# Performance work log

Measured on AMD Instinct MI355X. Metric: run time of the kernel, lower is better.

Reference implementation:

```python
import jax, jax.numpy as jnp
import numpy as np

N_NODES = 50000
N_EDGES = 600000
D = 128


def sage_conv(x, edge_index, Wl, bl, Wr):
    # PyG SAGEConv (mean aggr): out = lin_l(mean_{j in N(i)} x_j) + lin_r(x_i)
    src, dst = edge_index[0], edge_index[1]
    msgs = x[src]  # [E, D] gather of neighbor features
    summed = jax.ops.segment_sum(msgs, dst, num_segments=N_NODES)  # [N, D]
    deg = jax.ops.segment_sum(jnp.ones((msgs.shape[0],), x.dtype), dst, num_segments=N_NODES)
    mean = summed / jnp.maximum(deg, 1.0)[:, None]
    return mean @ Wl.T + bl + x @ Wr.T


def setup_inputs() -> dict:
    key = jax.random.key(0)
    ks = jax.random.split(key, 12)
    s = 1.0 / np.sqrt(D)
    inp = {
        "x": jax.random.normal(ks[0], (N_NODES, D), dtype=jnp.float32),
        "edge_index": jax.random.randint(ks[1], (2, N_EDGES), 0, N_NODES, dtype=jnp.int64),
    }
    for i, layer in enumerate([1, 2, 3]):
        inp[f"Wl{layer}"] = jax.random.uniform(ks[2 + 3 * i], (D, D), jnp.float32, -s, s)
        inp[f"bl{layer}"] = jax.random.uniform(ks[3 + 3 * i], (D,), jnp.float32, -s, s)
        inp[f"Wr{layer}"] = jax.random.uniform(ks[4 + 3 * i], (D, D), jnp.float32, -s, s)
    return inp


def reference(x, edge_index, Wl1, bl1, Wr1, Wl2, bl2, Wr2, Wl3, bl3, Wr3):
    h = jax.nn.relu(sage_conv(x, edge_index, Wl1, bl1, Wr1))
    h = jax.nn.relu(sage_conv(h, edge_index, Wl2, bl2, Wr2))
    h = jax.nn.relu(sage_conv(h, edge_index, Wl3, bl3, Wr3))
    return h
```

## Files before the change

### kernel.cpp

```cpp
#include <hip/hip_runtime.h>
#include <hip/hip_bf16.h>
#include <stdint.h>

#define N_NODES 50000
#define N_EDGES 600000
#define DD 128
#define K2 256
#define M_PAD 50048
#define MAXDEG 64
#define NREP 4
#define SEGCAP 16
#define POISON 0xAAAAAAAAu

#define FILL_BLOCKS 2344
#define PREP_BLOCKS 3125

typedef __bf16 bf16x8 __attribute__((ext_vector_type(8)));
typedef float floatx4 __attribute__((ext_vector_type(4)));

__device__ __forceinline__ ushort f2bf(float f) {
    union { float f; uint u; } v; v.f = f;
    uint u = v.u;
    u += 0x7fffu + ((u >> 16) & 1u);
    return (ushort)(u >> 16);
}
__device__ __forceinline__ float bf2f(ushort h) {
    union { uint u; float f; } v; v.u = ((uint)h) << 16;
    return v.f;
}
__device__ __forceinline__ void accum8(float* a, uint4 p) {
    a[0] += bf2f((ushort)(p.x & 0xffffu)); a[1] += bf2f((ushort)(p.x >> 16));
    a[2] += bf2f((ushort)(p.y & 0xffffu)); a[3] += bf2f((ushort)(p.y >> 16));
    a[4] += bf2f((ushort)(p.z & 0xffffu)); a[5] += bf2f((ushort)(p.z >> 16));
    a[6] += bf2f((ushort)(p.w & 0xffffu)); a[7] += bf2f((ushort)(p.w >> 16));
}
__device__ __forceinline__ uint4 packf8(float4 f0, float4 f1) {
    uint4 o;
    o.x = (uint)f2bf(f0.x) | ((uint)f2bf(f0.y) << 16);
    o.y = (uint)f2bf(f0.z) | ((uint)f2bf(f0.w) << 16);
    o.z = (uint)f2bf(f1.x) | ((uint)f2bf(f1.y) << 16);
    o.w = (uint)f2bf(f1.z) | ((uint)f2bf(f1.w) << 16);
    return o;
}


__global__ void k_build(const float* __restrict__ x, ushort* __restrict__ X,
                        uint* __restrict__ cursor, ushort* __restrict__ col,
                        const int* __restrict__ eidx,
                        const float* __restrict__ Wl1, const float* __restrict__ Wr1,
                        const float* __restrict__ Wl2, const float* __restrict__ Wr2,
                        const float* __restrict__ Wl3, const float* __restrict__ Wr3,
                        ushort* __restrict__ Wb) {
    if (blockIdx.x < FILL_BLOCKS) {
        int t = blockIdx.x * 256 + threadIdx.x;
        if (t >= N_EDGES) return;
        int src = eidx[t];
        int dst = eidx[N_EDGES + t];
        int r = t & (NREP - 1);
        uint o = atomicAdd(&cursor[(size_t)dst * NREP + r], 1u) - POISON;
        if (o < SEGCAP) col[dst * MAXDEG + r * SEGCAP + o] = (ushort)src;
    } else {
        int idx = (blockIdx.x - FILL_BLOCKS) * 256 + threadIdx.x;
        if (idx < 3 * DD * K2 / 8) {
            int l = idx >> 12;
            int r = idx & 4095;
            int j = r >> 5, c = (r & 31) * 8;
            const float* Wl = (l == 0) ? Wl1 : (l == 1) ? Wl2 : Wl3;
            const float* Wr = (l == 0) ? Wr1 : (l == 1) ? Wr2 : Wr3;
            const float* W = (c < DD) ? &Wl[j * DD + c] : &Wr[j * DD + c - DD];
            float4 f0 = *(const float4*)W;
            float4 f1 = *(const float4*)(W + 4);
            *(uint4*)&Wb[(size_t)l * DD * K2 + j * K2 + c] = packf8(f0, f1);
        }
        if (idx >= N_NODES * 16) return;
        int i = idx >> 4, c = (idx & 15) * 8;
        float4 f0 = *(const float4*)&x[(size_t)i * DD + c];
        float4 f1 = *(const float4*)&x[(size_t)i * DD + c + 4];
        *(uint4*)&X[(size_t)i * DD + c] = packf8(f0, f1);
    }
}


__global__ void k_agg(const ushort* __restrict__ X, ushort* __restrict__ M,
                      const uint* __restrict__ cursor, const ushort* __restrict__ colell) {
    int wid = (blockIdx.x * blockDim.x + threadIdx.x) >> 6;
    if (wid >= N_NODES) return;
    int lane = threadIdx.x & 63;
    int sg = lane >> 4, l16 = lane & 15;

    uint4 c4 = *(const uint4*)&cursor[(size_t)wid * NREP];
    int d0 = (int)min(c4.x - POISON, (uint)SEGCAP);
    int d1 = (int)min(c4.y - POISON, (uint)SEGCAP);
    int d2 = (int)min(c4.z - POISON, (uint)SEGCAP);
    int d3 = (int)min(c4.w - POISON, (uint)SEGCAP);
    int deg = d0 + d1 + d2 + d3;
    int dr = (sg == 0) ? d0 : (sg == 1) ? d1 : (sg == 2) ? d2 : d3;
    int pre = ((sg > 0) ? d0 : 0) + ((sg > 1) ? d1 : 0) + ((sg > 2) ? d2 : 0);
    int nb = (int)colell[wid * MAXDEG + lane];
    int dstb = ((l16 < dr) ? (pre + l16) : 63) * 4;
    nb = __builtin_amdgcn_ds_permute(dstb, nb);

    float a[8] = {0, 0, 0, 0, 0, 0, 0, 0};
    const int choff = l16 * 8;
    int dm1 = deg - 1;
    for (int base = 0; base < deg; base += 16) {
        int i0 = base + sg, i1 = i0 + 4, i2 = i0 + 8, i3 = i0 + 12;
        int s0 = __shfl(nb, min(i0, dm1), 64);
        int s1 = __shfl(nb, min(i1, dm1), 64);
        int s2 = __shfl(nb, min(i2, dm1), 64);
        int s3 = __shfl(nb, min(i3, dm1), 64);
        uint4 p0 = *(const uint4*)&X[(size_t)s0 * DD + choff];
        uint4 p1 = *(const uint4*)&X[(size_t)s1 * DD + choff];
        uint4 p2 = *(const uint4*)&X[(size_t)s2 * DD + choff];
        uint4 p3 = *(const uint4*)&X[(size_t)s3 * DD + choff];
        if (i0 < deg) accum8(a, p0);
        if (i1 < deg) accum8(a, p1);
        if (i2 < deg) accum8(a, p2);
        if (i3 < deg) accum8(a, p3);
    }
    float inv = 1.0f / (float)max(deg, 1);
    #pragma unroll
    for (int j = 0; j < 8; ++j) {
        float v = a[j];
        v += __shfl_xor(v, 16, 64);
        v += __shfl_xor(v, 32, 64);
        a[j] = v * inv;
    }
    if (lane < 16) {
        uint4 o;
        o.x = (uint)f2bf(a[0]) | ((uint)f2bf(a[1]) << 16);
        o.y = (uint)f2bf(a[2]) | ((uint)f2bf(a[3]) << 16);
        o.z = (uint)f2bf(a[4]) | ((uint)f2bf(a[5]) << 16);
        o.w = (uint)f2bf(a[6]) | ((uint)f2bf(a[7]) << 16);
        *(uint4*)&M[(size_t)wid * DD + l16 * 8] = o;
    }
}


template <bool LAST>
__global__ __launch_bounds__(256) void k_gemm(const ushort* __restrict__ M,
                                              const ushort* __restrict__ Xin,
                                              const ushort* __restrict__ Wb,
                                              const float* __restrict__ bias,
                                              ushort* __restrict__ Xout,
                                              float* __restrict__ out) {
    __shared__ ushort As[64 * 72];
    __shared__ ushort Bs[128 * 72];
    int tid = threadIdx.x;
    int wave = tid >> 6, lane = tid & 63;
    int quad = lane >> 4, l16 = lane & 15;
    int i0 = blockIdx.x * 64;

    floatx4 acc[8];
    #pragma unroll
    for (int ct = 0; ct < 8; ++ct) acc[ct] = (floatx4){0.f, 0.f, 0.f, 0.f};

    for (int kb = 0; kb < K2; kb += 64) {
        const ushort* Asrc = (kb < DD) ? M : Xin;
        int kbase = kb & (DD - 1);
        __syncthreads();
        for (int it = 0; it < 2; ++it) {
            int idx = tid + it * 256;
            int r = idx >> 3, c = (idx & 7) * 8;
            *(uint4*)&As[r * 72 + c] =
                *(const uint4*)&Asrc[(size_t)(i0 + r) * DD + kbase + c];
        }
        for (int it = 0; it < 4; ++it) {
            int idx = tid + it * 256;
            int j = idx >> 3, c = (idx & 7) * 8;
            *(uint4*)&Bs[j * 72 + c] = *(const uint4*)&Wb[j * K2 + kb + c];
        }
        __syncthreads();
        for (int ks = 0; ks < 64; ks += 32) {
            bf16x8 a = *(const bf16x8*)&As[(wave * 16 + l16) * 72 + ks + quad * 8];
            #pragma unroll
            for (int ct = 0; ct < 8; ++ct) {
                bf16x8 b = *(const bf16x8*)&Bs[(ct * 16 + l16) * 72 + ks + quad * 8];
                acc[ct] = __builtin_amdgcn_mfma_f32_16x16x32_bf16(a, b, acc[ct], 0, 0, 0);
            }
        }
    }
    #pragma unroll
    for (int ct = 0; ct < 8; ++ct) {
        int colg = ct * 16 + l16;
        float bv = bias[colg];
        #pragma unroll
        for (int r = 0; r < 4; ++r) {
            int row = i0 + wave * 16 + quad * 4 + r;
            if (row < N_NODES) {
                float v = fmaxf(acc[ct][r] + bv, 0.0f);
                if (LAST)
                    out[(size_t)row * DD + colg] = v;
                else
                    Xout[(size_t)row * DD + colg] = f2bf(v);
            }
        }
    }
}


extern "C" void kernel_launch(void* const* d_in, const int* in_sizes, int n_in,
                              void* d_out, int out_size, void* d_ws, size_t ws_size,
                              hipStream_t stream) {
    const float* x = (const float*)d_in[0];
    const int* eidx = (const int*)d_in[1];

    char* ws = (char*)d_ws;
    size_t off = 0;
    auto alloc = [&](size_t bytes) {
        void* p = ws + off;
        off += (bytes + 255) & ~(size_t)255;
        return p;
    };
    ushort* X = (ushort*)alloc((size_t)M_PAD * DD * 2);
    ushort* M = (ushort*)alloc((size_t)M_PAD * DD * 2);
    uint* cursor = (uint*)alloc((size_t)M_PAD * NREP * 4);
    ushort* col = (ushort*)alloc((size_t)M_PAD * MAXDEG * 2);
    ushort* Wb = (ushort*)alloc((size_t)3 * DD * K2 * 2);
    (void)ws_size;

    k_build<<<FILL_BLOCKS + PREP_BLOCKS, 256, 0, stream>>>(
        x, X, cursor, col, eidx,
        (const float*)d_in[2], (const float*)d_in[4],
        (const float*)d_in[5], (const float*)d_in[7],
        (const float*)d_in[8], (const float*)d_in[10], Wb);

    const int aggGrid = (N_NODES * 64 + 255) / 256;
    const int gemmGrid = M_PAD / 64;

    for (int l = 0; l < 3; ++l) {
        const float* bl = (const float*)d_in[3 + 3 * l];
        const ushort* WbL = Wb + (size_t)l * DD * K2;
        k_agg<<<aggGrid, 256, 0, stream>>>(X, M, cursor, col);
        if (l < 2)
            k_gemm<false><<<gemmGrid, 256, 0, stream>>>(M, X, WbL, bl, X, nullptr);
        else
            k_gemm<true><<<gemmGrid, 256, 0, stream>>>(M, X, WbL, bl, nullptr, (float*)d_out);
    }
}
```

Measured before the change: 244.3 us.

## Fuse neighbor mean aggregation into the per-layer GEMM kernel

Each layer now runs one kernel that aggregates neighbor features for its 64-node tile into shared memory and then performs the MFMA GEMM directly from it. The self-feature operand is held in registers, and X is ping-ponged between two buffers. This removes the intermediate M round trip through global memory and half the kernel launches. The trade-off is that aggregation now iterates 16 nodes serially per wave with far fewer waves in flight, which can reduce latency hiding for the random gathers.

```diff
diff --git a/kernel.cpp b/kernel.cpp
--- a/kernel.cpp
+++ b/kernel.cpp
@@ -81,105 +81,116 @@
 }
 
 
-__global__ void k_agg(const ushort* __restrict__ X, ushort* __restrict__ M,
-                      const uint* __restrict__ cursor, const ushort* __restrict__ colell) {
-    int wid = (blockIdx.x * blockDim.x + threadIdx.x) >> 6;
-    if (wid >= N_NODES) return;
-    int lane = threadIdx.x & 63;
-    int sg = lane >> 4, l16 = lane & 15;
-
-    uint4 c4 = *(const uint4*)&cursor[(size_t)wid * NREP];
-    int d0 = (int)min(c4.x - POISON, (uint)SEGCAP);
-    int d1 = (int)min(c4.y - POISON, (uint)SEGCAP);
-    int d2 = (int)min(c4.z - POISON, (uint)SEGCAP);
-    int d3 = (int)min(c4.w - POISON, (uint)SEGCAP);
-    int deg = d0 + d1 + d2 + d3;
-    int dr = (sg == 0) ? d0 : (sg == 1) ? d1 : (sg == 2) ? d2 : d3;
-    int pre = ((sg > 0) ? d0 : 0) + ((sg > 1) ? d1 : 0) + ((sg > 2) ? d2 : 0);
-    int nb = (int)colell[wid * MAXDEG + lane];
-    int dstb = ((l16 < dr) ? (pre + l16) : 63) * 4;
-    nb = __builtin_amdgcn_ds_permute(dstb, nb);
-
-    float a[8] = {0, 0, 0, 0, 0, 0, 0, 0};
-    const int choff = l16 * 8;
-    int dm1 = deg - 1;
-    for (int base = 0; base < deg; base += 16) {
-        int i0 = base + sg, i1 = i0 + 4, i2 = i0 + 8, i3 = i0 + 12;
-        int s0 = __shfl(nb, min(i0, dm1), 64);
-        int s1 = __shfl(nb, min(i1, dm1), 64);
-        int s2 = __shfl(nb, min(i2, dm1), 64);
-        int s3 = __shfl(nb, min(i3, dm1), 64);
-        uint4 p0 = *(const uint4*)&X[(size_t)s0 * DD + choff];
-        uint4 p1 = *(const uint4*)&X[(size_t)s1 * DD + choff];
-        uint4 p2 = *(const uint4*)&X[(size_t)s2 * DD + choff];
-        uint4 p3 = *(const uint4*)&X[(size_t)s3 * DD + choff];
-        if (i0 < deg) accum8(a, p0);
-        if (i1 < deg) accum8(a, p1);
-        if (i2 < deg) accum8(a, p2);
-        if (i3 < deg) accum8(a, p3);
-    }
-    float inv = 1.0f / (float)max(deg, 1);
-    #pragma unroll
-    for (int j = 0; j < 8; ++j) {
-        float v = a[j];
-        v += __shfl_xor(v, 16, 64);
-        v += __shfl_xor(v, 32, 64);
-        a[j] = v * inv;
-    }
-    if (lane < 16) {
-        uint4 o;
-        o.x = (uint)f2bf(a[0]) | ((uint)f2bf(a[1]) << 16);
-        o.y = (uint)f2bf(a[2]) | ((uint)f2bf(a[3]) << 16);
-        o.z = (uint)f2bf(a[4]) | ((uint)f2bf(a[5]) << 16);
-        o.w = (uint)f2bf(a[6]) | ((uint)f2bf(a[7]) << 16);
-        *(uint4*)&M[(size_t)wid * DD + l16 * 8] = o;
-    }
-}
-
-
 template <bool LAST>
-__global__ __launch_bounds__(256) void k_gemm(const ushort* __restrict__ M,
-                                              const ushort* __restrict__ Xin,
-                                              const ushort* __restrict__ Wb,
-                                              const float* __restrict__ bias,
-                                              ushort* __restrict__ Xout,
-                                              float* __restrict__ out) {
-    __shared__ ushort As[64 * 72];
+__global__ __launch_bounds__(256) void k_fused(const ushort* __restrict__ Xin,
+                                               const ushort* __restrict__ Wb,
+                                               const float* __restrict__ bias,
+                                               const uint* __restrict__ cursor,
+                                               const ushort* __restrict__ colell,
+                                               ushort* __restrict__ Xout,
+                                               float* __restrict__ out) {
+    __shared__ ushort Ms[64 * 136];
     __shared__ ushort Bs[128 * 72];
     int tid = threadIdx.x;
     int wave = tid >> 6, lane = tid & 63;
     int quad = lane >> 4, l16 = lane & 15;
     int i0 = blockIdx.x * 64;
 
+    uint4 xr0, xr1, xr2, xr3;
+    {
+        const ushort* xrow = &Xin[(size_t)(i0 + wave * 16 + l16) * DD + quad * 8];
+        xr0 = *(const uint4*)&xrow[0];
+        xr1 = *(const uint4*)&xrow[32];
+        xr2 = *(const uint4*)&xrow[64];
+        xr3 = *(const uint4*)&xrow[96];
+    }
+
+    const int choff = l16 * 8;
+    #pragma unroll 2
+    for (int t = 0; t < 16; ++t) {
+        int node = i0 + wave * 16 + t;
+        uint4 c4 = *(const uint4*)&cursor[(size_t)node * NREP];
+        int d0 = (int)min(c4.x - POISON, (uint)SEGCAP);
+        int d1 = (int)min(c4.y - POISON, (uint)SEGCAP);
+        int d2 = (int)min(c4.z - POISON, (uint)SEGCAP);
+        int d3 = (int)min(c4.w - POISON, (uint)SEGCAP);
+        int deg = d0 + d1 + d2 + d3;
+        int dr = (quad == 0) ? d0 : (quad == 1) ? d1 : (quad == 2) ? d2 : d3;
+        int pre = ((quad > 0) ? d0 : 0) + ((quad > 1) ? d1 : 0) + ((quad > 2) ? d2 : 0);
+        int nb = (int)colell[node * MAXDEG + lane];
+        int dstb = ((l16 < dr) ? (pre + l16) : 63) * 4;
+        nb = __builtin_amdgcn_ds_permute(dstb, nb);
+
+        float a[8] = {0, 0, 0, 0, 0, 0, 0, 0};
+        int dm1 = deg - 1;
+        for (int base = 0; base < deg; base += 16) {
+            int ii0 = base + quad, ii1 = ii0 + 4, ii2 = ii0 + 8, ii3 = ii0 + 12;
+            int s0 = __shfl(nb, min(ii0, dm1), 64);
+            int s1 = __shfl(nb, min(ii1, dm1), 64);
+            int s2 = __shfl(nb, min(ii2, dm1), 64);
+            int s3 = __shfl(nb, min(ii3, dm1), 64);
+            uint4 p0 = *(const uint4*)&Xin[(size_t)s0 * DD + choff];
+            uint4 p1 = *(const uint4*)&Xin[(size_t)s1 * DD + choff];
+            uint4 p2 = *(const uint4*)&Xin[(size_t)s2 * DD + choff];
+            uint4 p3 = *(const uint4*)&Xin[(size_t)s3 * DD + choff];
+            if (ii0 < deg) accum8(a, p0);
+            if (ii1 < deg) accum8(a, p1);
+            if (ii2 < deg) accum8(a, p2);
+            if (ii3 < deg) accum8(a, p3);
+        }
+        float inv = 1.0f / (float)max(deg, 1);
+        #pragma unroll
+        for (int j = 0; j < 8; ++j) {
+            float v = a[j];
+            v += __shfl_xor(v, 16, 64);
+            v += __shfl_xor(v, 32, 64);
+            a[j] = v * inv;
+        }
+        if (lane < 16) {
+            uint4 o;
+            o.x = (uint)f2bf(a[0]) | ((uint)f2bf(a[1]) << 16);
+            o.y = (uint)f2bf(a[2]) | ((uint)f2bf(a[3]) << 16);
+            o.z = (uint)f2bf(a[4]) | ((uint)f2bf(a[5]) << 16);
+            o.w = (uint)f2bf(a[6]) | ((uint)f2bf(a[7]) << 16);
+            *(uint4*)&Ms[(wave * 16 + t) * 136 + l16 * 8] = o;
+        }
+    }
+    __syncthreads();
+
     floatx4 acc[8];
     #pragma unroll
     for (int ct = 0; ct < 8; ++ct) acc[ct] = (floatx4){0.f, 0.f, 0.f, 0.f};
 
-    for (int kb = 0; kb < K2; kb += 64) {
-        const ushort* Asrc = (kb < DD) ? M : Xin;
-        int kbase = kb & (DD - 1);
-        __syncthreads();
-        for (int it = 0; it < 2; ++it) {
-            int idx = tid + it * 256;
-            int r = idx >> 3, c = (idx & 7) * 8;
-            *(uint4*)&As[r * 72 + c] =
-                *(const uint4*)&Asrc[(size_t)(i0 + r) * DD + kbase + c];
-        }
+    #pragma unroll
+    for (int kbi = 0; kbi < 4; ++kbi) {
+        int kb = kbi * 64;
         for (int it = 0; it < 4; ++it) {
             int idx = tid + it * 256;
             int j = idx >> 3, c = (idx & 7) * 8;
             *(uint4*)&Bs[j * 72 + c] = *(const uint4*)&Wb[j * K2 + kb + c];
         }
         __syncthreads();
-        for (int ks = 0; ks < 64; ks += 32) {
-            bf16x8 a = *(const bf16x8*)&As[(wave * 16 + l16) * 72 + ks + quad * 8];
+        #pragma unroll
+        for (int ksi = 0; ksi < 2; ++ksi) {
+            int ks = ksi * 32;
+            bf16x8 av;
+            if (kbi < 2) {
+                av = *(const bf16x8*)&Ms[(wave * 16 + l16) * 136 + kb + ks + quad * 8];
+            } else {
+                union { uint4 u; bf16x8 v; } cvt;
+                cvt.u = (kbi == 2) ? (ksi == 0 ? xr0 : xr1)
+                                   : (ksi == 0 ? xr2 : xr3);
+                av = cvt.v;
+            }
             #pragma unroll
             for (int ct = 0; ct < 8; ++ct) {
                 bf16x8 b = *(const bf16x8*)&Bs[(ct * 16 + l16) * 72 + ks + quad * 8];
-                acc[ct] = __builtin_amdgcn_mfma_f32_16x16x32_bf16(a, b, acc[ct], 0, 0, 0);
+                acc[ct] = __builtin_amdgcn_mfma_f32_16x16x32_bf16(av, b, acc[ct], 0, 0, 0);
             }
         }
-    }
+        __syncthreads();
+    }
+
     #pragma unroll
     for (int ct = 0; ct < 8; ++ct) {
         int colg = ct * 16 + l16;
@@ -212,29 +223,26 @@
         off += (bytes + 255) & ~(size_t)255;
         return p;
     };
-    ushort* X = (ushort*)alloc((size_t)M_PAD * DD * 2);
-    ushort* M = (ushort*)alloc((size_t)M_PAD * DD * 2);
+    ushort* X0 = (ushort*)alloc((size_t)M_PAD * DD * 2);
+    ushort* X1 = (ushort*)alloc((size_t)M_PAD * DD * 2);
     uint* cursor = (uint*)alloc((size_t)M_PAD * NREP * 4);
     ushort* col = (ushort*)alloc((size_t)M_PAD * MAXDEG * 2);
     ushort* Wb = (ushort*)alloc((size_t)3 * DD * K2 * 2);
     (void)ws_size;
 
     k_build<<<FILL_BLOCKS + PREP_BLOCKS, 256, 0, stream>>>(
-        x, X, cursor, col, eidx,
+        x, X0, cursor, col, eidx,
         (const float*)d_in[2], (const float*)d_in[4],
         (const float*)d_in[5], (const float*)d_in[7],
         (const float*)d_in[8], (const float*)d_in[10], Wb);
 
-    const int aggGrid = (N_NODES * 64 + 255) / 256;
-    const int gemmGrid = M_PAD / 64;
-
-    for (int l = 0; l < 3; ++l) {
-        const float* bl = (const float*)d_in[3 + 3 * l];
-        const ushort* WbL = Wb + (size_t)l * DD * K2;
-        k_agg<<<aggGrid, 256, 0, stream>>>(X, M, cursor, col);
-        if (l < 2)
-            k_gemm<false><<<gemmGrid, 256, 0, stream>>>(M, X, WbL, bl, X, nullptr);
-        else
-            k_gemm<true><<<gemmGrid, 256, 0, stream>>>(M, X, WbL, bl, nullptr, (float*)d_out);
-    }
-}
+    const int grid = M_PAD / 64;
+
+    k_fused<false><<<grid, 256, 0, stream>>>(
+        X0, Wb, (const float*)d_in[3], cursor, col, X1, nullptr);
+    k_fused<false><<<grid, 256, 0, stream>>>(
+        X1, Wb + (size_t)DD * K2, (const float*)d_in[6], cursor, col, X0, nullptr);
+    k_fused<true><<<grid, 256, 0, stream>>>(
+        X0, Wb + (size_t)2 * DD * K2, (const float*)d_in[9], cursor, col,
+        nullptr, (float*)d_out);
+}
```

Result: slower. 250.6 us (+2.6%).
